# Kernel tuning notes

Hardware: AMD Instinct MI355X
Metric: run time of the kernel (lower is better)

## Reference

```python
import jax, jax.numpy as jnp
import numpy as np

N = 100000   # nodes (single node type 'A')
C = 256      # hidden_channels
OUT = 128    # out_channels
E_RAND = 300000  # random edges; total E = N + E_RAND = 400000
LN_EPS = 1e-5


def _linear_params(key, in_c, out_c):
    kw, kb = jax.random.split(key)
    bound = 1.0 / np.sqrt(in_c)
    W = jax.random.uniform(kw, (out_c, in_c), minval=-bound, maxval=bound, dtype=jnp.float32)
    b = jax.random.uniform(kb, (out_c,), minval=-bound, maxval=bound, dtype=jnp.float32)
    return W, b


def _edges(key):
    # guarantee every node appears in both rows -> unique()/remap in the torch
    # code is the identity, so the subgraph equals the full graph
    k0, k1 = jax.random.split(key)
    base = jnp.arange(N, dtype=jnp.int64)
    row0 = jnp.concatenate([base, jax.random.randint(k0, (E_RAND,), 0, N, dtype=jnp.int64)])
    row1 = jnp.concatenate([base, jax.random.randint(k1, (E_RAND,), 0, N, dtype=jnp.int64)])
    return jnp.stack([row0, row1])


def setup_inputs() -> dict:
    key = jax.random.key(0)
    ks = jax.random.split(key, 12)
    x = jax.random.normal(ks[0], (N, C), dtype=jnp.float32)
    edge_index_r0 = _edges(ks[1])
    edge_index_r1 = _edges(ks[2])
    wl0, bl0 = _linear_params(ks[3], C, C)
    w00, b00 = _linear_params(ks[4], C, C)
    w10, b10 = _linear_params(ks[5], C, C)
    wl1, bl1 = _linear_params(ks[6], C, C)
    w01, b01 = _linear_params(ks[7], C, C)
    w11, b11 = _linear_params(ks[8], C, C)
    Wout, bout = _linear_params(ks[9], C, OUT)
    return dict(
        x=x, edge_index_r0=edge_index_r0, edge_index_r1=edge_index_r1,
        wl0=wl0, bl0=bl0, w00=w00, b00=b00, w10=w10, b10=b10,
        gate0=jnp.float32(0.5), lns0=jnp.ones((C,), jnp.float32), lnb0=jnp.zeros((C,), jnp.float32),
        wl1=wl1, bl1=bl1, w01=w01, b01=b01, w11=w11, b11=b11,
        gate1=jnp.float32(0.5), lns1=jnp.ones((C,), jnp.float32), lnb1=jnp.zeros((C,), jnp.float32),
        Wout=Wout, bout=bout,
    )


def _metapath_layer(x0, h, ei, wl, bl, w0, b0, w1, b1, gate, lns, lnb):
    n = h.shape[0]
    src, dst = ei[0], ei[1]
    # PyG flow='target_to_source', aggr='add': message x_j = h[edge_index[1]],
    # scatter-added at edge_index[0]
    agg = jax.ops.segment_sum(h[dst], src, num_segments=n)
    # original code normalizes by bincount of edge_index[1] (kept faithfully)
    deg = jax.ops.segment_sum(jnp.ones_like(dst, dtype=h.dtype), dst, num_segments=n)
    agg = agg / jnp.clip(deg, 1.0)[:, None]
    g = jax.nn.sigmoid(gate)
    out = (agg @ wl.T + bl) + (1.0 - g) * (h @ w0.T + b0) + g * (x0 @ w1.T + b1)
    out = jax.nn.relu(out)
    mu = out.mean(-1, keepdims=True)
    var = out.var(-1, keepdims=True)
    out = (out - mu) / jnp.sqrt(var + LN_EPS) * lns + lnb
    return out  # dropout is identity in eval mode


def reference(x, edge_index_r0, edge_index_r1,
              wl0, bl0, w00, b00, w10, b10, gate0, lns0, lnb0,
              wl1, bl1, w01, b01, w11, b11, gate1, lns1, lnb1,
              Wout, bout):
    x0 = jax.lax.stop_gradient(x)  # x0_dict is detached in the torch code
    h = x
    # metapath is processed in reverse: conv index 1 first, then conv index 0
    h = _metapath_layer(x0, h, edge_index_r1, wl1, bl1, w01, b01, w11, b11, gate1, lns1, lnb1)
    h = _metapath_layer(x0, h, edge_index_r0, wl0, bl0, w00, b00, w10, b10, gate0, lns0, lnb0)
    return h @ Wout.T + bout
```

## Files before the change

### kernel.cpp

```cpp
#include <hip/hip_runtime.h>

typedef unsigned short u16;
typedef unsigned int   u32;

typedef __attribute__((ext_vector_type(8))) __bf16 bf16x8;
typedef __attribute__((ext_vector_type(8))) unsigned short u16x8;
typedef __attribute__((ext_vector_type(4))) float  f32x4;

#define C      256
#define OUTC   128
#define LN_EPS 1e-5f

__device__ __forceinline__ float bf2f(u16 u) {
    u32 i = ((u32)u) << 16; float f; __builtin_memcpy(&f, &i, 4); return f;
}
__device__ __forceinline__ u16 f2bf(float f) {
    u32 i; __builtin_memcpy(&i, &f, 4);
    u32 r = (i + 0x7FFFu + ((i >> 16) & 1u)) >> 16;
    return (u16)r;
}
__device__ __forceinline__ void load_lds16(const void* g, void* l) {
    __builtin_amdgcn_global_load_lds((const __attribute__((address_space(1))) u32*)g,
                                     (__attribute__((address_space(3))) u32*)l, 16, 0, 0);
}
__device__ __forceinline__ int swz(int row) { return (row + (row >> 2)) & 3; }

#define PREP_BLK 1408
__global__ void prep_combo(const float* wl0, const float* w00, const float* w10,
                           const float* bl0, const float* b00, const float* b10,
                           const float* gate0,
                           const float* wl1, const float* w01, const float* w11,
                           const float* bl1, const float* b01, const float* b11,
                           const float* gate1,
                           const float* Wout, const float* x,
                           u16* __restrict__ WcatA, u16* __restrict__ WcatB,
                           u16* __restrict__ Woutb, float* __restrict__ bcat,
                           u16* __restrict__ xb, size_t n8)
{
    if (blockIdx.x >= PREP_BLK) {
        size_t i = ((size_t)(blockIdx.x - PREP_BLK) * 256 + threadIdx.x);
        if (i >= n8) return;
        const float* p = x + i * 8;
        float4 v0 = *(const float4*)p;
        float4 v1 = *(const float4*)(p + 4);
        u16x8 o;
        o[0] = f2bf(v0.x); o[1] = f2bf(v0.y); o[2] = f2bf(v0.z); o[3] = f2bf(v0.w);
        o[4] = f2bf(v1.x); o[5] = f2bf(v1.y); o[6] = f2bf(v1.z); o[7] = f2bf(v1.w);
        *(u16x8*)(xb + i * 8) = o;
        return;
    }
    int idx = blockIdx.x * 256 + threadIdx.x;
    float gA = 1.f / (1.f + expf(-gate1[0]));
    float gB = 1.f / (1.f + expf(-gate0[0]));
    if (idx < 256 * 512) {
        int n = idx >> 9, k = idx & 511;
        float v;
        if (k < 256) v = wl1[n * 256 + k];
        else         v = (1.f - gA) * w01[n * 256 + (k - 256)] + gA * w11[n * 256 + (k - 256)];
        WcatA[idx] = f2bf(v);
    } else if (idx < 256 * 512 + 256 * 768) {
        int j = idx - 256 * 512;
        int n = j / 768, k = j - n * 768;
        float v;
        if (k < 256)      v = wl0[n * 256 + k];
        else if (k < 512) v = (1.f - gB) * w00[n * 256 + (k - 256)];
        else              v = gB * w10[n * 256 + (k - 512)];
        WcatB[j] = f2bf(v);
    } else {
        int j = idx - (256 * 512 + 256 * 768);
        if (j < OUTC * C) Woutb[j] = f2bf(Wout[j]);
    }
    if (idx < 512) {
        int nn = idx & 255;
        if (idx < 256) bcat[idx] = bl1[nn] + (1.f - gA) * b01[nn] + gA * b11[nn];
        else           bcat[idx] = bl0[nn] + (1.f - gB) * b00[nn] + gB * b10[nn];
    }
}

__global__ void count_edges2(const int* __restrict__ ei1, const int* __restrict__ ei0,
                             int* __restrict__ cnt1, int* __restrict__ deg1,
                             int* __restrict__ cnt0, int* __restrict__ deg0,
                             int E, int Nn, int ebg)
{
    int b = blockIdx.x;
    const int* ei; int *cnt, *deg;
    if (b < ebg) { ei = ei1; cnt = cnt1; deg = deg1; }
    else         { b -= ebg; ei = ei0; cnt = cnt0; deg = deg0; }
    int idx = b * 256 + threadIdx.x;
    if (idx >= E) return;
    int s = ei[idx], d = ei[E + idx];
    if ((unsigned)s >= (unsigned)Nn || (unsigned)d >= (unsigned)Nn) return;
    atomicAdd(cnt + s, 1);
    atomicAdd(deg + d, 1);
}

__global__ void block_sums2(const int* __restrict__ cnt1, const int* __restrict__ cnt0,
                            int* __restrict__ parts1, int* __restrict__ parts0,
                            int n, int nblk)
{
    int b = blockIdx.x;
    const int* counts; int* partials;
    if (b < nblk) { counts = cnt1; partials = parts1; }
    else          { b -= nblk; counts = cnt0; partials = parts0; }
    int i = b * 256 + threadIdx.x;
    int v = (i < n) ? counts[i] : 0;
    #pragma unroll
    for (int off = 32; off; off >>= 1) v += __shfl_down(v, off, 64);
    __shared__ int ws[4];
    if ((threadIdx.x & 63) == 0) ws[threadIdx.x >> 6] = v;
    __syncthreads();
    if (threadIdx.x == 0) partials[b] = ws[0] + ws[1] + ws[2] + ws[3];
}

__global__ void scan_partials2(int* __restrict__ parts1, int* __restrict__ parts0, int nblk)
{
    int* partials = blockIdx.x ? parts0 : parts1;
    __shared__ int buf[1024];
    int tid = threadIdx.x;
    int v = (tid < nblk) ? partials[tid] : 0;
    buf[tid] = v; __syncthreads();
    for (int off = 1; off < 1024; off <<= 1) {
        int t = (tid >= off) ? buf[tid - off] : 0;
        __syncthreads();
        buf[tid] += t;
        __syncthreads();
    }
    if (tid < nblk) partials[tid] = buf[tid] - v;
}

__global__ void make_offsets2(int* __restrict__ cnt1, int* __restrict__ cnt0,
                              const int* __restrict__ parts1, const int* __restrict__ parts0,
                              int* __restrict__ off1a, int* __restrict__ off0a,
                              int n, int nblk)
{
    int b = blockIdx.x;
    int* counts_cursor; const int* partials; int* offsets;
    if (b < nblk) { counts_cursor = cnt1; partials = parts1; offsets = off1a; }
    else          { b -= nblk; counts_cursor = cnt0; partials = parts0; offsets = off0a; }
    __shared__ int buf[256];
    int i = b * 256 + threadIdx.x;
    int cnt = (i < n) ? counts_cursor[i] : 0;
    buf[threadIdx.x] = cnt; __syncthreads();
    for (int off = 1; off < 256; off <<= 1) {
        int t = (threadIdx.x >= off) ? buf[threadIdx.x - off] : 0;
        __syncthreads();
        buf[threadIdx.x] += t;
        __syncthreads();
    }
    int off = partials[b] + buf[threadIdx.x] - cnt;
    if (i < n) {
        offsets[i] = off;
        counts_cursor[i] = off;
        if (i == n - 1) offsets[n] = off + cnt;
    }
}

__global__ void fill_edges2(const int* __restrict__ ei1, const int* __restrict__ ei0,
                            int* __restrict__ cur1, int* __restrict__ cur0,
                            int* __restrict__ ed1, int* __restrict__ ed0,
                            int E, int Nn, int ebg)
{
    int b = blockIdx.x;
    const int* ei; int *cursor, *edgedst;
    if (b < ebg) { ei = ei1; cursor = cur1; edgedst = ed1; }
    else         { b -= ebg; ei = ei0; cursor = cur0; edgedst = ed0; }
    int idx = b * 256 + threadIdx.x;
    if (idx >= E) return;
    int s = ei[idx], d = ei[E + idx];
    if ((unsigned)s >= (unsigned)Nn || (unsigned)d >= (unsigned)Nn) return;
    int p = atomicAdd(cursor + s, 1);
    edgedst[p] = d;
}

__global__ __launch_bounds__(256) void gather_kernel(
    const int* __restrict__ offsets, const int* __restrict__ edgedst,
    const int* __restrict__ degcnt, const u16* __restrict__ h,
    u16* __restrict__ aggb, int Nn)
{
    int node = blockIdx.x * 4 + (threadIdx.x >> 6);
    if (node >= Nn) return;
    int lane = threadIdx.x & 63;
    int beg = offsets[node], end = offsets[node + 1];
    float4 a0 = {0.f, 0.f, 0.f, 0.f}, a1 = {0.f, 0.f, 0.f, 0.f};
    int e = beg;
    for (; e + 1 < end; e += 2) {
        int d0 = edgedst[e], d1 = edgedst[e + 1];
        ushort4 v0 = *(const ushort4*)(h + (size_t)d0 * C + lane * 4);
        ushort4 v1 = *(const ushort4*)(h + (size_t)d1 * C + lane * 4);
        a0.x += bf2f(v0.x); a0.y += bf2f(v0.y); a0.z += bf2f(v0.z); a0.w += bf2f(v0.w);
        a1.x += bf2f(v1.x); a1.y += bf2f(v1.y); a1.z += bf2f(v1.z); a1.w += bf2f(v1.w);
    }
    if (e < end) {
        int d0 = edgedst[e];
        ushort4 v0 = *(const ushort4*)(h + (size_t)d0 * C + lane * 4);
        a0.x += bf2f(v0.x); a0.y += bf2f(v0.y); a0.z += bf2f(v0.z); a0.w += bf2f(v0.w);
    }
    float inv = 1.0f / fmaxf((float)degcnt[node], 1.0f);
    ushort4 o;
    o.x = f2bf((a0.x + a1.x) * inv); o.y = f2bf((a0.y + a1.y) * inv);
    o.z = f2bf((a0.z + a1.z) * inv); o.w = f2bf((a0.w + a1.w) * inv);
    *(ushort4*)(aggb + (size_t)node * C + lane * 4) = o;
}

template <int NSEG>
__global__ __launch_bounds__(512, 4) void layer_gemm(
    const u16* __restrict__ s0, const u16* __restrict__ s1, const u16* __restrict__ s2,
    const u16* __restrict__ W,
    const float* __restrict__ bcat,
    const float* __restrict__ lns, const float* __restrict__ lnb,
    u16* __restrict__ Hout, int Nnodes)
{
    constexpr int WK = NSEG * 256;
    constexpr int KT = NSEG * 8;

    __shared__ u16 Alds[128 * 32];
    __shared__ u16 Blds[256 * 32];
    __shared__ float lnpart[128][4][2];

    const int tid  = threadIdx.x;
    const int wave = tid >> 6, lane = tid & 63;
    const int wave_m = wave & 1, wave_n = wave >> 1;
    const int q = lane >> 4, l15 = lane & 15;
    const int m0 = blockIdx.x * 128;

    const int srow = (wave << 4) + (lane >> 2);
    int anode = m0 + srow; if (anode >= Nnodes) anode = Nnodes - 1;
    const int asc = (lane & 3) ^ swz(srow);
    const size_t a_goff = (size_t)anode * C + asc * 8;
    u16* a_ldst = Alds + (wave << 9);

    const u16* bgp[2]; u16* bldst[2];
    #pragma unroll
    for (int i = 0; i < 2; ++i) {
        int cb = wave + i * 8;
        int brow = (cb << 4) + (lane >> 2);
        int bsc = (lane & 3) ^ swz(brow);
        bgp[i]   = W + brow * WK + bsc * 8;
        bldst[i] = Blds + (cb << 9);
    }

    int aoff[4], boff[4];
    #pragma unroll
    for (int t = 0; t < 4; ++t) {
        int ar = wave_m * 64 + t * 16 + l15;
        aoff[t] = ar * 32 + ((q ^ swz(ar)) << 3);
        int br = wave_n * 64 + t * 16 + l15;
        boff[t] = br * 32 + ((q ^ swz(br)) << 3);
    }

    f32x4 acc[4][4] = {};

    for (int kt = 0; kt < KT; ++kt) {
        const u16* Asrc = (kt < 8) ? s0 : ((NSEG == 2 || kt < 16) ? s1 : s2);
        load_lds16(Asrc + a_goff + ((kt & 7) << 5), a_ldst);
        int k0 = kt << 5;
        load_lds16(bgp[0] + k0, bldst[0]);
        load_lds16(bgp[1] + k0, bldst[1]);
        __syncthreads();

        bf16x8 af[4], bfr[4];
        #pragma unroll
        for (int t = 0; t < 4; ++t) af[t]  = *(const bf16x8*)&Alds[aoff[t]];
        #pragma unroll
        for (int f = 0; f < 4; ++f) bfr[f] = *(const bf16x8*)&Blds[boff[f]];
        #pragma unroll
        for (int t = 0; t < 4; ++t)
            #pragma unroll
            for (int f = 0; f < 4; ++f)
                acc[t][f] = __builtin_amdgcn_mfma_f32_16x16x32_bf16(af[t], bfr[f], acc[t][f], 0, 0, 0);
        __syncthreads();
    }

    float bias[4], lsc[4], lbi[4];
    #pragma unroll
    for (int f = 0; f < 4; ++f) {
        int n = wave_n * 64 + f * 16 + l15;
        bias[f] = bcat[n]; lsc[f] = lns[n]; lbi[f] = lnb[n];
    }
    #pragma unroll
    for (int t = 0; t < 4; ++t)
        #pragma unroll
        for (int r = 0; r < 4; ++r) {
            float p = 0.f, pp = 0.f;
            #pragma unroll
            for (int f = 0; f < 4; ++f) {
                float v = acc[t][f][r] + bias[f];
                v = fmaxf(v, 0.f);
                acc[t][f][r] = v;
                p += v; pp += v * v;
            }
            #pragma unroll
            for (int off = 1; off < 16; off <<= 1) {
                p  += __shfl_xor(p,  off, 16);
                pp += __shfl_xor(pp, off, 16);
            }
            if (l15 == 0) {
                int row = wave_m * 64 + t * 16 + q * 4 + r;
                lnpart[row][wave_n][0] = p;
                lnpart[row][wave_n][1] = pp;
            }
        }
    __syncthreads();
    #pragma unroll
    for (int t = 0; t < 4; ++t)
        #pragma unroll
        for (int r = 0; r < 4; ++r) {
            int row = wave_m * 64 + t * 16 + q * 4 + r;
            int node = m0 + row;
            if (node < Nnodes) {
                float S1 = lnpart[row][0][0] + lnpart[row][1][0]
                         + lnpart[row][2][0] + lnpart[row][3][0];
                float S2 = lnpart[row][0][1] + lnpart[row][1][1]
                         + lnpart[row][2][1] + lnpart[row][3][1];
                float mean = S1 * (1.f / 256.f);
                float var  = fmaxf(S2 * (1.f / 256.f) - mean * mean, 0.f);
                float rstd = rsqrtf(var + LN_EPS);
                u16* op = Hout + (size_t)node * C;
                #pragma unroll
                for (int f = 0; f < 4; ++f) {
                    int n = wave_n * 64 + f * 16 + l15;
                    op[n] = f2bf((acc[t][f][r] - mean) * rstd * lsc[f] + lbi[f]);
                }
            }
        }
}

__global__ __launch_bounds__(512, 4) void final_gemm(
    const u16* __restrict__ A, const u16* __restrict__ W,
    const float* __restrict__ bout, float* __restrict__ out, int Nnodes)
{
    __shared__ u16 Alds[128 * 32];
    __shared__ u16 Blds[128 * 32];

    const int tid = threadIdx.x;
    const int wave = tid >> 6, lane = tid & 63;
    const int wave_m = wave & 1, wave_n = wave >> 1;
    const int q = lane >> 4, l15 = lane & 15;
    const int m0 = blockIdx.x * 128;

    const int srow = (wave << 4) + (lane >> 2);
    int anode = m0 + srow; if (anode >= Nnodes) anode = Nnodes - 1;
    const int asc = (lane & 3) ^ swz(srow);
    const size_t a_goff = (size_t)anode * C + asc * 8;
    u16* a_ldst = Alds + (wave << 9);

    const int bsc = (lane & 3) ^ swz(srow);
    const u16* bgp = W + srow * C + bsc * 8;
    u16* bldst = Blds + (wave << 9);

    int aoff[4], boff[2];
    #pragma unroll
    for (int t = 0; t < 4; ++t) {
        int ar = wave_m * 64 + t * 16 + l15;
        aoff[t] = ar * 32 + ((q ^ swz(ar)) << 3);
    }
    #pragma unroll
    for (int f = 0; f < 2; ++f) {
        int br = wave_n * 32 + f * 16 + l15;
        boff[f] = br * 32 + ((q ^ swz(br)) << 3);
    }

    f32x4 acc[4][2] = {};

    for (int kt = 0; kt < 8; ++kt) {
        int k0 = kt << 5;
        load_lds16(A + a_goff + k0, a_ldst);
        load_lds16(bgp + k0, bldst);
        __syncthreads();

        bf16x8 af[4], bfr[2];
        #pragma unroll
        for (int t = 0; t < 4; ++t) af[t]  = *(const bf16x8*)&Alds[aoff[t]];
        #pragma unroll
        for (int f = 0; f < 2; ++f) bfr[f] = *(const bf16x8*)&Blds[boff[f]];
        #pragma unroll
        for (int t = 0; t < 4; ++t)
            #pragma unroll
            for (int f = 0; f < 2; ++f)
                acc[t][f] = __builtin_amdgcn_mfma_f32_16x16x32_bf16(af[t], bfr[f], acc[t][f], 0, 0, 0);
        __syncthreads();
    }

    float bias[2];
    #pragma unroll
    for (int f = 0; f < 2; ++f) bias[f] = bout[wave_n * 32 + f * 16 + l15];
    #pragma unroll
    for (int t = 0; t < 4; ++t)
        #pragma unroll
        for (int r = 0; r < 4; ++r) {
            int row = wave_m * 64 + t * 16 + q * 4 + r;
            int node = m0 + row;
            if (node < Nnodes) {
                float* op = out + (size_t)node * OUTC;
                #pragma unroll
                for (int f = 0; f < 2; ++f) {
                    int n = wave_n * 32 + f * 16 + l15;
                    op[n] = acc[t][f][r] + bias[f];
                }
            }
        }
}

extern "C" void kernel_launch(void* const* d_in, const int* in_sizes, int n_in,
                              void* d_out, int out_size, void* d_ws, size_t ws_size,
                              hipStream_t stream)
{
    const float* x    = (const float*)d_in[0];
    const int*   ei0  = (const int*)d_in[1];
    const int*   ei1  = (const int*)d_in[2];
    const float* wl0  = (const float*)d_in[3];
    const float* bl0  = (const float*)d_in[4];
    const float* w00  = (const float*)d_in[5];
    const float* b00  = (const float*)d_in[6];
    const float* w10  = (const float*)d_in[7];
    const float* b10  = (const float*)d_in[8];
    const float* gate0= (const float*)d_in[9];
    const float* lns0 = (const float*)d_in[10];
    const float* lnb0 = (const float*)d_in[11];
    const float* wl1  = (const float*)d_in[12];
    const float* bl1  = (const float*)d_in[13];
    const float* w01  = (const float*)d_in[14];
    const float* b01  = (const float*)d_in[15];
    const float* w11  = (const float*)d_in[16];
    const float* b11  = (const float*)d_in[17];
    const float* gate1= (const float*)d_in[18];
    const float* lns1 = (const float*)d_in[19];
    const float* lnb1 = (const float*)d_in[20];
    const float* Wout = (const float*)d_in[21];
    const float* bout = (const float*)d_in[22];

    const int N = in_sizes[0] / C;
    const int E = in_sizes[1] / 2;

    char* w = (char*)d_ws;
    u16*   WcatA = (u16*)w;   w += (size_t)256 * 512 * 2;
    u16*   WcatB = (u16*)w;   w += (size_t)256 * 768 * 2;
    u16*   Woutb = (u16*)w;   w += (size_t)OUTC * C * 2;
    float* bcat  = (float*)w; w += 4096;
    int*   cnt1  = (int*)w;   w += (size_t)N * 4;
    int*   deg1  = (int*)w;   w += (size_t)N * 4;
    int*   cnt0  = (int*)w;   w += (size_t)N * 4;
    int*   deg0  = (int*)w;   w += (size_t)N * 4;
    int*   off1  = (int*)w;   w += (((size_t)(N + 1) * 4) + 255) & ~255ull;
    int*   off0  = (int*)w;   w += (((size_t)(N + 1) * 4) + 255) & ~255ull;
    int*   parts1= (int*)w;   w += 4096;
    int*   parts0= (int*)w;   w += 4096;
    int*   ed1   = (int*)w;   w += (size_t)E * 4;
    int*   ed0   = (int*)w;   w += (size_t)E * 4;
    u16*   xb    = (u16*)w;   w += (size_t)N * C * 2;
    u16*   aggb  = (u16*)w;   w += (size_t)N * C * 2;
    u16*   h1    = (u16*)w;   w += (size_t)N * C * 2;

    const int eb_grid = (E + 255) / 256;
    const int nblk    = (N + 255) / 256;
    const int gt_grid = (N + 3) / 4;
    const int gm_grid = (N + 127) / 128;
    const size_t n8   = (size_t)N * C / 8;
    const int xc_blk  = (int)((n8 + 255) / 256);
    u16* h2 = (u16*)d_out;

    hipMemsetAsync(cnt1, 0, (size_t)4 * N * 4, stream);
    prep_combo<<<PREP_BLK + xc_blk, 256, 0, stream>>>(
        wl0, w00, w10, bl0, b00, b10, gate0,
        wl1, w01, w11, bl1, b01, b11, gate1,
        Wout, x, WcatA, WcatB, Woutb, bcat, xb, n8);

    count_edges2 <<<2 * eb_grid, 256, 0, stream>>>(ei1, ei0, cnt1, deg1, cnt0, deg0, E, N, eb_grid);
    block_sums2  <<<2 * nblk, 256, 0, stream>>>(cnt1, cnt0, parts1, parts0, N, nblk);
    scan_partials2<<<2, 1024, 0, stream>>>(parts1, parts0, nblk);
    make_offsets2<<<2 * nblk, 256, 0, stream>>>(cnt1, cnt0, parts1, parts0, off1, off0, N, nblk);
    fill_edges2  <<<2 * eb_grid, 256, 0, stream>>>(ei1, ei0, cnt1, cnt0, ed1, ed0, E, N, eb_grid);

    gather_kernel<<<gt_grid, 256, 0, stream>>>(off1, ed1, deg1, xb, aggb, N);
    layer_gemm<2><<<gm_grid, 512, 0, stream>>>(aggb, xb, nullptr, WcatA, bcat,
                                               lns1, lnb1, h1, N);

    gather_kernel<<<gt_grid, 256, 0, stream>>>(off0, ed0, deg0, h1, aggb, N);
    layer_gemm<3><<<gm_grid, 512, 0, stream>>>(aggb, h1, xb, WcatB, bcat + C,
                                               lns0, lnb0, h2, N);

    final_gemm<<<gm_grid, 512, 0, stream>>>(h2, Woutb, bout, (float*)d_out, N);
}
```

Before: 548.2 us.

## Double-buffer LDS tiles in layer and final GEMM kernels

Adds a second LDS buffer for the A and B tiles in both GEMM kernels. The global-to-LDS load for the next k-step is issued before the MFMA work on the current one, so load latency overlaps compute. The cost is double the LDS use per block, which may lower occupancy at 512 threads with launch bounds of 4 blocks. There is also a subtle sync concern: the load into buffer 1 for the next step is issued before the barrier, right after buffer 1 was read in the previous iteration. That is safe only because a barrier ends each iteration.

```diff
diff --git a/kernel.cpp b/kernel.cpp
--- a/kernel.cpp
+++ b/kernel.cpp
@@ -213,8 +213,8 @@
     constexpr int WK = NSEG * 256;
     constexpr int KT = NSEG * 8;
 
-    __shared__ u16 Alds[128 * 32];
-    __shared__ u16 Blds[256 * 32];
+    __shared__ u16 Alds[2][128 * 32];
+    __shared__ u16 Blds[2][256 * 32];
     __shared__ float lnpart[128][4][2];
 
     const int tid  = threadIdx.x;
@@ -227,16 +227,16 @@
     int anode = m0 + srow; if (anode >= Nnodes) anode = Nnodes - 1;
     const int asc = (lane & 3) ^ swz(srow);
     const size_t a_goff = (size_t)anode * C + asc * 8;
-    u16* a_ldst = Alds + (wave << 9);
-
-    const u16* bgp[2]; u16* bldst[2];
+    const int a_lo = wave << 9;
+
+    const u16* bgp[2]; int b_lo[2];
     #pragma unroll
     for (int i = 0; i < 2; ++i) {
         int cb = wave + i * 8;
         int brow = (cb << 4) + (lane >> 2);
         int bsc = (lane & 3) ^ swz(brow);
-        bgp[i]   = W + brow * WK + bsc * 8;
-        bldst[i] = Blds + (cb << 9);
+        bgp[i]  = W + brow * WK + bsc * 8;
+        b_lo[i] = cb << 9;
     }
 
     int aoff[4], boff[4];
@@ -250,24 +250,34 @@
 
     f32x4 acc[4][4] = {};
 
-    for (int kt = 0; kt < KT; ++kt) {
+    auto stage = [&](int b, int kt) {
         const u16* Asrc = (kt < 8) ? s0 : ((NSEG == 2 || kt < 16) ? s1 : s2);
-        load_lds16(Asrc + a_goff + ((kt & 7) << 5), a_ldst);
+        load_lds16(Asrc + a_goff + ((kt & 7) << 5), &Alds[b][a_lo]);
         int k0 = kt << 5;
-        load_lds16(bgp[0] + k0, bldst[0]);
-        load_lds16(bgp[1] + k0, bldst[1]);
-        __syncthreads();
-
+        load_lds16(bgp[0] + k0, &Blds[b][b_lo[0]]);
+        load_lds16(bgp[1] + k0, &Blds[b][b_lo[1]]);
+    };
+    auto compute = [&](const u16* __restrict__ Ab, const u16* __restrict__ Bb) {
         bf16x8 af[4], bfr[4];
         #pragma unroll
-        for (int t = 0; t < 4; ++t) af[t]  = *(const bf16x8*)&Alds[aoff[t]];
-        #pragma unroll
-        for (int f = 0; f < 4; ++f) bfr[f] = *(const bf16x8*)&Blds[boff[f]];
+        for (int t = 0; t < 4; ++t) af[t]  = *(const bf16x8*)(Ab + aoff[t]);
+        #pragma unroll
+        for (int f = 0; f < 4; ++f) bfr[f] = *(const bf16x8*)(Bb + boff[f]);
         #pragma unroll
         for (int t = 0; t < 4; ++t)
             #pragma unroll
             for (int f = 0; f < 4; ++f)
                 acc[t][f] = __builtin_amdgcn_mfma_f32_16x16x32_bf16(af[t], bfr[f], acc[t][f], 0, 0, 0);
+    };
+
+    stage(0, 0);
+    __syncthreads();
+    for (int kt = 0; kt < KT; kt += 2) {
+        stage(1, kt + 1);
+        compute(&Alds[0][0], &Blds[0][0]);
+        __syncthreads();
+        if (kt + 2 < KT) stage(0, kt + 2);
+        compute(&Alds[1][0], &Blds[1][0]);
         __syncthreads();
     }
 
@@ -329,8 +339,8 @@
     const u16* __restrict__ A, const u16* __restrict__ W,
     const float* __restrict__ bout, float* __restrict__ out, int Nnodes)
 {
-    __shared__ u16 Alds[128 * 32];
-    __shared__ u16 Blds[128 * 32];
+    __shared__ u16 Alds[2][128 * 32];
+    __shared__ u16 Blds[2][128 * 32];
 
     const int tid = threadIdx.x;
     const int wave = tid >> 6, lane = tid & 63;
@@ -342,11 +352,11 @@
     int anode = m0 + srow; if (anode >= Nnodes) anode = Nnodes - 1;
     const int asc = (lane & 3) ^ swz(srow);
     const size_t a_goff = (size_t)anode * C + asc * 8;
-    u16* a_ldst = Alds + (wave << 9);
+    const int a_lo = wave << 9;
 
     const int bsc = (lane & 3) ^ swz(srow);
     const u16* bgp = W + srow * C + bsc * 8;
-    u16* bldst = Blds + (wave << 9);
+    const int b_lo = wave << 9;
 
     int aoff[4], boff[2];
     #pragma unroll
@@ -362,22 +372,32 @@
 
     f32x4 acc[4][2] = {};
 
-    for (int kt = 0; kt < 8; ++kt) {
+    auto stage = [&](int b, int kt) {
         int k0 = kt << 5;
-        load_lds16(A + a_goff + k0, a_ldst);
-        load_lds16(bgp + k0, bldst);
-        __syncthreads();
-
+        load_lds16(A + a_goff + k0, &Alds[b][a_lo]);
+        load_lds16(bgp + k0, &Blds[b][b_lo]);
+    };
+    auto compute = [&](const u16* __restrict__ Ab, const u16* __restrict__ Bb) {
         bf16x8 af[4], bfr[2];
         #pragma unroll
-        for (int t = 0; t < 4; ++t) af[t]  = *(const bf16x8*)&Alds[aoff[t]];
-        #pragma unroll
-        for (int f = 0; f < 2; ++f) bfr[f] = *(const bf16x8*)&Blds[boff[f]];
+        for (int t = 0; t < 4; ++t) af[t]  = *(const bf16x8*)(Ab + aoff[t]);
+        #pragma unroll
+        for (int f = 0; f < 2; ++f) bfr[f] = *(const bf16x8*)(Bb + boff[f]);
         #pragma unroll
         for (int t = 0; t < 4; ++t)
             #pragma unroll
             for (int f = 0; f < 2; ++f)
                 acc[t][f] = __builtin_amdgcn_mfma_f32_16x16x32_bf16(af[t], bfr[f], acc[t][f], 0, 0, 0);
+    };
+
+    stage(0, 0);
+    __syncthreads();
+    for (int kt = 0; kt < 8; kt += 2) {
+        stage(1, kt + 1);
+        compute(&Alds[0][0], &Blds[0][0]);
+        __syncthreads();
+        if (kt + 2 < 8) stage(0, kt + 2);
+        compute(&Alds[1][0], &Blds[1][0]);
         __syncthreads();
     }
 
```

New measurement: 551.7 us. About the same (+0.6%).
